# Kernel tuning notes

Measured on AMD Instinct MI355X. Metric: run time of the kernel, lower is better.

Reference implementation:

```python
import jax, jax.numpy as jnp
import numpy as np

FRAME_T = 8
NUM_K = 10


def _masked_att(att, temp):
    # att: [B, H, P, P] -> softmax over groups of size P//FRAME_T, top-k threshold mask
    B, H, P, _ = att.shape
    D = P // FRAME_T
    a = att.reshape(B, H, P, FRAME_T, D)
    a = jax.nn.softmax(a / temp, axis=-1)
    # k-th largest value per row as threshold (torch.topk values are sorted desc)
    margin = jax.lax.top_k(a, NUM_K)[0][..., -1]  # [B,H,P,FRAME_T]
    a = a * (a >= margin[..., None])
    return a  # [B,H,P,FRAME_T,D]


def setup_inputs() -> dict:
    key = jax.random.key(0)
    k1, k2, k3, k4 = jax.random.split(key, 4)
    B, H, P, hd = 4, 12, 1568, 64
    return {
        "att_s": jax.random.normal(k1, (B, H, P, P), dtype=jnp.float32),
        "att_t": jax.random.normal(k2, (B, H, P, P), dtype=jnp.float32),
        "v_s": jax.random.normal(k3, (B, H, P, hd), dtype=jnp.float32),
        "v_t": jax.random.normal(k4, (B, H, P, hd), dtype=jnp.float32),
    }


def reference(att_s, att_t, v_s, v_t):
    temp = jnp.float32(1.0)
    B, H, P, _ = att_t.shape
    H_s = att_s.shape[1]
    h_dim = v_t.shape[-1]
    D = P // FRAME_T

    a_s = _masked_att(att_s, temp)  # [B,Hs,P,T,D]
    a_t = _masked_att(att_t, temp)  # [B,H,P,T,D]

    vt = v_t.reshape(B, H, D, FRAME_T, h_dim)
    vs = v_s.reshape(B, H_s, D, FRAME_T, h_dim)

    norm_s = a_s.sum(-1)  # [B,Hs,P,T]
    norm_t = a_t.sum(-1)

    o_s = jnp.einsum('bhptd,bhdte->bhpte', a_s, vs) / norm_s[..., None]
    o_t = jnp.einsum('bhptd,bhdte->bhpte', a_t, vt) / norm_t[..., None]

    loss = jnp.mean((o_s - o_t) ** 2)
    return loss
```

## Files before the change

### kernel.cpp

```cpp
#include <hip/hip_runtime.h>
#include <hip/hip_bf16.h>

#define PP 1568
#define TT 8
#define DD 196
#define HD 64
#define NBH 48
#define NROW (NBH*PP*TT)
#define RPB 32
#define NBLK3 (NROW/RPB)
#define NRED1 ((NBLK3+255)/256)
#define SUB (8*DD*4)
#define VSLAB (DD*TT*HD)
#define BPB 392
#define KMASK 0xFFFFFF00u

typedef float f4 __attribute__((ext_vector_type(4)));
typedef unsigned u4v __attribute__((ext_vector_type(4)));

__device__ __forceinline__ float readlane_f(float v, int l) {
    return __int_as_float(__builtin_amdgcn_readlane(__float_as_int(v), l));
}

__device__ __forceinline__ float wave_sum_u(float v) {
#define STEPS(ctrl) { float t_ = __int_as_float(__builtin_amdgcn_update_dpp( \
        0, __float_as_int(v), ctrl, 0xF, 0xF, true)); v += t_; }
    STEPS(0x111) STEPS(0x112) STEPS(0x114) STEPS(0x118) STEPS(0x142) STEPS(0x143)
#undef STEPS
    return readlane_f(v, 63);
}

__device__ __forceinline__ unsigned UMX(unsigned a, unsigned b){ return a>b?a:b; }
__device__ __forceinline__ unsigned UMN(unsigned a, unsigned b){ return a<b?a:b; }

__device__ __forceinline__ unsigned med3u(unsigned a, unsigned b, unsigned c) {
    unsigned d;
    asm("v_med3_u32 %0, %1, %2, %3" : "=v"(d) : "v"(a), "v"(b), "v"(c));
    return d;
}

__device__ __forceinline__ float untr(unsigned u) {
    return (u & 0x80000000u) ? __uint_as_float(u ^ 0x80000000u)
                             : __uint_as_float(~u);
}

struct K6  { unsigned k0,k1,k2,k3,k4,k5; };
struct K10 { unsigned k0,k1,k2,k3,k4,k5,k6,k7,k8,k9; };
struct MR  { K10 f; unsigned mx; };

#define PUTK6(Q,X,D) { unsigned b_=__float_as_uint(X); \
  unsigned u_=b_^((unsigned)((int)b_>>31)|0x80000000u); \
  unsigned c_=(u_&KMASK)|(unsigned)(D); \
  unsigned n0_=UMX(Q.k0,c_); \
  unsigned n1_=med3u(Q.k0,Q.k1,c_); \
  unsigned n2_=med3u(Q.k1,Q.k2,c_); \
  unsigned n3_=med3u(Q.k2,Q.k3,c_); \
  unsigned n4_=med3u(Q.k3,Q.k4,c_); \
  unsigned n5_=med3u(Q.k4,Q.k5,c_); \
  Q.k0=n0_; Q.k1=n1_; Q.k2=n2_; Q.k3=n3_; Q.k4=n4_; Q.k5=n5_; }
#define PUT4K6(Q,V,D0) PUTK6(Q,(V).x,(D0)) PUTK6(Q,(V).y,(D0)+1) \
                       PUTK6(Q,(V).z,(D0)+2) PUTK6(Q,(V).w,(D0)+3)

__device__ __forceinline__ K6 chain_rows(const char* stg, int a, int b8) {
    K6 q = {0,0,0,0,0,0};
    const char* rb = stg + a*784 + b8*16;
    f4 v;
    v = *(const f4*)(rb);       PUT4K6(q, v, b8*4)
    v = *(const f4*)(rb+128);   PUT4K6(q, v, b8*4+32)
    v = *(const f4*)(rb+256);   PUT4K6(q, v, b8*4+64)
    v = *(const f4*)(rb+384);   PUT4K6(q, v, b8*4+96)
    v = *(const f4*)(rb+512);   PUT4K6(q, v, b8*4+128)
    v = *(const f4*)(rb+640);   PUT4K6(q, v, b8*4+160)
    if (b8 == 7) { v = *(const f4*)(stg + a*784 + 768); PUT4K6(q, v, 192) }
    return q;
}

#define SWZ(x, pat) (unsigned)__builtin_amdgcn_ds_swizzle((int)(x), pat)
__device__ __forceinline__ K6 kshuf8_6(K6 a) {
    K6 r;
    r.k0=SWZ(a.k0,0x201F); r.k1=SWZ(a.k1,0x201F); r.k2=SWZ(a.k2,0x201F);
    r.k3=SWZ(a.k3,0x201F); r.k4=SWZ(a.k4,0x201F); r.k5=SWZ(a.k5,0x201F);
    return r;
}
__device__ __forceinline__ K10 kshuf16(K10 a) {
    K10 r;
    r.k0=SWZ(a.k0,0x401F); r.k1=SWZ(a.k1,0x401F); r.k2=SWZ(a.k2,0x401F);
    r.k3=SWZ(a.k3,0x401F); r.k4=SWZ(a.k4,0x401F); r.k5=SWZ(a.k5,0x401F);
    r.k6=SWZ(a.k6,0x401F); r.k7=SWZ(a.k7,0x401F); r.k8=SWZ(a.k8,0x401F);
    r.k9=SWZ(a.k9,0x401F);
    return r;
}
__device__ __forceinline__ K10 kbp32(K10 a, int bpx) {
    K10 r;
    r.k0=(unsigned)__builtin_amdgcn_ds_bpermute(bpx,(int)a.k0);
    r.k1=(unsigned)__builtin_amdgcn_ds_bpermute(bpx,(int)a.k1);
    r.k2=(unsigned)__builtin_amdgcn_ds_bpermute(bpx,(int)a.k2);
    r.k3=(unsigned)__builtin_amdgcn_ds_bpermute(bpx,(int)a.k3);
    r.k4=(unsigned)__builtin_amdgcn_ds_bpermute(bpx,(int)a.k4);
    r.k5=(unsigned)__builtin_amdgcn_ds_bpermute(bpx,(int)a.k5);
    r.k6=(unsigned)__builtin_amdgcn_ds_bpermute(bpx,(int)a.k6);
    r.k7=(unsigned)__builtin_amdgcn_ds_bpermute(bpx,(int)a.k7);
    r.k8=(unsigned)__builtin_amdgcn_ds_bpermute(bpx,(int)a.k8);
    r.k9=(unsigned)__builtin_amdgcn_ds_bpermute(bpx,(int)a.k9);
    return r;
}

__device__ __forceinline__ K10 kmrg66(K6 A, K6 B) {
    unsigned p00=UMN(A.k0,B.k0);
    unsigned p01=UMN(A.k0,B.k1), p10=UMN(A.k1,B.k0);
    unsigned p02=UMN(A.k0,B.k2), p11=UMN(A.k1,B.k1), p20=UMN(A.k2,B.k0);
    unsigned p03=UMN(A.k0,B.k3), p12=UMN(A.k1,B.k2), p21=UMN(A.k2,B.k1), p30=UMN(A.k3,B.k0);
    unsigned p04=UMN(A.k0,B.k4), p13=UMN(A.k1,B.k3), p22=UMN(A.k2,B.k2), p31=UMN(A.k3,B.k1), p40=UMN(A.k4,B.k0);
    unsigned p05=UMN(A.k0,B.k5), p14=UMN(A.k1,B.k4), p23=UMN(A.k2,B.k3), p32=UMN(A.k3,B.k2), p41=UMN(A.k4,B.k1), p50=UMN(A.k5,B.k0);
    unsigned p15=UMN(A.k1,B.k5), p24=UMN(A.k2,B.k4), p33=UMN(A.k3,B.k3), p42=UMN(A.k4,B.k2), p51=UMN(A.k5,B.k1);
    unsigned p25=UMN(A.k2,B.k5), p34=UMN(A.k3,B.k4), p43=UMN(A.k4,B.k3), p52=UMN(A.k5,B.k2);
    unsigned p35=UMN(A.k3,B.k5), p44=UMN(A.k4,B.k4), p53=UMN(A.k5,B.k3);
    K10 M;
    M.k0=UMX(A.k0,B.k0);
    M.k1=UMX(UMX(A.k1,B.k1),p00);
    M.k2=UMX(UMX(A.k2,B.k2),UMX(p01,p10));
    M.k3=UMX(UMX(A.k3,B.k3),UMX(p02,UMX(p11,p20)));
    M.k4=UMX(UMX(A.k4,B.k4),UMX(UMX(p03,p12),UMX(p21,p30)));
    M.k5=UMX(UMX(A.k5,B.k5),UMX(UMX(p04,p13),UMX(p22,UMX(p31,p40))));
    M.k6=UMX(UMX(p05,p14),UMX(UMX(p23,p32),UMX(p41,p50)));
    M.k7=UMX(UMX(p15,p24),UMX(p33,UMX(p42,p51)));
    M.k8=UMX(UMX(p25,p34),UMX(p43,p52));
    M.k9=UMX(p35,UMX(p44,p53));
    return M;
}

__device__ __forceinline__ K10 kmrg(K10 A, K10 B) {
    unsigned p00=UMN(A.k0,B.k0);
    unsigned p01=UMN(A.k0,B.k1), p10=UMN(A.k1,B.k0);
    unsigned p02=UMN(A.k0,B.k2), p11=UMN(A.k1,B.k1), p20=UMN(A.k2,B.k0);
    unsigned p03=UMN(A.k0,B.k3), p12=UMN(A.k1,B.k2), p21=UMN(A.k2,B.k1), p30=UMN(A.k3,B.k0);
    unsigned p04=UMN(A.k0,B.k4), p13=UMN(A.k1,B.k3), p22=UMN(A.k2,B.k2), p31=UMN(A.k3,B.k1), p40=UMN(A.k4,B.k0);
    unsigned p05=UMN(A.k0,B.k5), p14=UMN(A.k1,B.k4), p23=UMN(A.k2,B.k3), p32=UMN(A.k3,B.k2), p41=UMN(A.k4,B.k1), p50=UMN(A.k5,B.k0);
    unsigned p06=UMN(A.k0,B.k6), p15=UMN(A.k1,B.k5), p24=UMN(A.k2,B.k4), p33=UMN(A.k3,B.k3), p42=UMN(A.k4,B.k2), p51=UMN(A.k5,B.k1), p60=UMN(A.k6,B.k0);
    unsigned p07=UMN(A.k0,B.k7), p16=UMN(A.k1,B.k6), p25=UMN(A.k2,B.k5), p34=UMN(A.k3,B.k4), p43=UMN(A.k4,B.k3), p52=UMN(A.k5,B.k2), p61=UMN(A.k6,B.k1), p70=UMN(A.k7,B.k0);
    unsigned p08=UMN(A.k0,B.k8), p17=UMN(A.k1,B.k7), p26=UMN(A.k2,B.k6), p35=UMN(A.k3,B.k5), p44=UMN(A.k4,B.k4), p53=UMN(A.k5,B.k3), p62=UMN(A.k6,B.k2), p71=UMN(A.k7,B.k1), p80=UMN(A.k8,B.k0);
    K10 M;
    M.k0=UMX(A.k0,B.k0);
    M.k1=UMX(UMX(A.k1,B.k1),p00);
    M.k2=UMX(UMX(A.k2,B.k2),UMX(p01,p10));
    M.k3=UMX(UMX(A.k3,B.k3),UMX(p02,UMX(p11,p20)));
    M.k4=UMX(UMX(A.k4,B.k4),UMX(UMX(p03,p12),UMX(p21,p30)));
    M.k5=UMX(UMX(A.k5,B.k5),UMX(UMX(p04,p13),UMX(p22,UMX(p31,p40))));
    M.k6=UMX(UMX(A.k6,B.k6),UMX(UMX(p05,p14),UMX(UMX(p23,p32),UMX(p41,p50))));
    M.k7=UMX(UMX(A.k7,B.k7),UMX(UMX(UMX(p06,p15),UMX(p24,p33)),UMX(UMX(p42,p51),p60)));
    M.k8=UMX(UMX(A.k8,B.k8),UMX(UMX(UMX(p07,p16),UMX(p25,p34)),UMX(UMX(p43,p52),UMX(p61,p70))));
    M.k9=UMX(UMX(A.k9,B.k9),UMX(UMX(UMX(p08,p17),UMX(p26,p35)),UMX(UMX(p44,p53),UMX(UMX(p62,p71),p80))));
    return M;
}

__device__ __forceinline__ MR merge_all(K6 q, int bpx) {
    K10 m = kmrg66(q, kshuf8_6(q));
    K10 n = kmrg(m, kshuf16(m));
    K10 r = kbp32(n, bpx);
    MR out;
    out.mx = UMX(n.k0, r.k0);
    out.f.k0=UMX(n.k0,r.k9); out.f.k1=UMX(n.k1,r.k8); out.f.k2=UMX(n.k2,r.k7);
    out.f.k3=UMX(n.k3,r.k6); out.f.k4=UMX(n.k4,r.k5); out.f.k5=UMX(n.k5,r.k4);
    out.f.k6=UMX(n.k6,r.k3); out.f.k7=UMX(n.k7,r.k2); out.f.k8=UMX(n.k8,r.k1);
    out.f.k9=UMX(n.k9,r.k0);
    return out;
}

#define LOADR(R, P) { const char* p_=(P); \
    R##0=*(const f4*)(p_+lane*16); \
    R##1=*(const f4*)(p_+1024+lane*16); \
    R##2=*(const f4*)(p_+2048+lane*16); \
    R##3=*(const f4*)(p_+3072+lane*16); \
    R##4=*(const f4*)(p_+4096+lane*16); \
    R##5=*(const f4*)(p_+5120+lane*16); \
    if (lane<8) R##6=*(const f4*)(p_+6144+lane*16); }
#define STORER(R) { \
    *(f4*)(stg+lane*16)=R##0; *(f4*)(stg+1024+lane*16)=R##1; \
    *(f4*)(stg+2048+lane*16)=R##2; *(f4*)(stg+3072+lane*16)=R##3; \
    *(f4*)(stg+4096+lane*16)=R##4; *(f4*)(stg+5120+lane*16)=R##5; \
    if (lane<8) *(f4*)(stg+6144+lane*16)=R##6; }

#define PKW(F,K) ((__float_as_uint(F)&KMASK)|((K)&0xFFu))

__global__ __launch_bounds__(64, 4) void vtop_main(
        const float* __restrict__ att_s, const float* __restrict__ att_t,
        const float* __restrict__ v_s,   const float* __restrict__ v_t,
        float* __restrict__ partial) {
    __shared__ f4  stgv[SUB/16];
    __shared__ u4v wbuf[5][RPB];
    char* stg = (char*)stgv;

    int lane = threadIdx.x;
    int blk  = blockIdx.x;
    int a = lane & 7, b8 = lane >> 3;
    int bpx = (lane ^ 32) << 2;

    const char* baseS = (const char*)att_s + (size_t)blk * (RPB*DD*4);
    const char* baseT = (const char*)att_t + (size_t)blk * (RPB*DD*4);

    f4 rs0{},rs1{},rs2{},rs3{},rs4{},rs5{},rs6{};
    f4 rt0{},rt1{},rt2{},rt3{},rt4{},rt5{},rt6{};

    LOADR(rs, baseS)

#pragma unroll 1
    for (int s = 0; s < 4; ++s) {
        STORER(rs)
        LOADR(rt, baseT + s*SUB)
        K6 qS = chain_rows(stg, a, b8);
        MR mS = merge_all(qS, bpx);
        STORER(rt)
        if (s < 3) LOADR(rs, baseS + (s+1)*SUB)
        K6 qT = chain_rows(stg, a, b8);
        MR mT = merge_all(qT, bpx);
        K10 fS = mS.f, fT = mT.f;

        float CS = untr(mS.mx & KMASK), CT = untr(mT.mx & KMASK);
        float wS0=__expf(untr(fS.k0&KMASK)-CS), wS1=__expf(untr(fS.k1&KMASK)-CS),
              wS2=__expf(untr(fS.k2&KMASK)-CS), wS3=__expf(untr(fS.k3&KMASK)-CS),
              wS4=__expf(untr(fS.k4&KMASK)-CS), wS5=__expf(untr(fS.k5&KMASK)-CS),
              wS6=__expf(untr(fS.k6&KMASK)-CS), wS7=__expf(untr(fS.k7&KMASK)-CS),
              wS8=__expf(untr(fS.k8&KMASK)-CS), wS9=__expf(untr(fS.k9&KMASK)-CS);
        float wT0=__expf(untr(fT.k0&KMASK)-CT), wT1=__expf(untr(fT.k1&KMASK)-CT),
              wT2=__expf(untr(fT.k2&KMASK)-CT), wT3=__expf(untr(fT.k3&KMASK)-CT),
              wT4=__expf(untr(fT.k4&KMASK)-CT), wT5=__expf(untr(fT.k5&KMASK)-CT),
              wT6=__expf(untr(fT.k6&KMASK)-CT), wT7=__expf(untr(fT.k7&KMASK)-CT),
              wT8=__expf(untr(fT.k8&KMASK)-CT), wT9=__expf(untr(fT.k9&KMASK)-CT);
        float wsS = (((wS0+wS1)+(wS2+wS3))+((wS4+wS5)+(wS6+wS7)))+(wS8+wS9);
        float wsT = (((wT0+wT1)+(wT2+wT3))+((wT4+wT5)+(wT6+wT7)))+(wT8+wT9);
        float invS =  __builtin_amdgcn_rcpf(wsS);
        float invT = -__builtin_amdgcn_rcpf(wsT);

        if (lane < 8) {
            int row = (s << 3) | lane;
            u4v w;
            w.x=PKW(wS0*invS,fS.k0); w.y=PKW(wS1*invS,fS.k1);
            w.z=PKW(wS2*invS,fS.k2); w.w=PKW(wS3*invS,fS.k3);
            wbuf[0][row]=w;
            w.x=PKW(wS4*invS,fS.k4); w.y=PKW(wS5*invS,fS.k5);
            w.z=PKW(wS6*invS,fS.k6); w.w=PKW(wS7*invS,fS.k7);
            wbuf[1][row]=w;
            w.x=PKW(wS8*invS,fS.k8); w.y=PKW(wS9*invS,fS.k9);
            w.z=PKW(wT0*invT,fT.k0); w.w=PKW(wT1*invT,fT.k1);
            wbuf[2][row]=w;
            w.x=PKW(wT2*invT,fT.k2); w.y=PKW(wT3*invT,fT.k3);
            w.z=PKW(wT4*invT,fT.k4); w.w=PKW(wT5*invT,fT.k5);
            wbuf[3][row]=w;
            w.x=PKW(wT6*invT,fT.k6); w.y=PKW(wT7*invT,fT.k7);
            w.z=PKW(wT8*invT,fT.k8); w.w=PKW(wT9*invT,fT.k9);
            wbuf[4][row]=w;
        }
    }

    int bh = blk / BPB;
    const float* vSb = v_s + (size_t)bh * VSLAB;
    const float* vTb = v_t + (size_t)bh * VSLAB;
    float lacc = 0.f;
#pragma unroll 1
    for (int k = 0; k < RPB; ++k) {
        unsigned base = ((unsigned)(k & 7) << 6) + (unsigned)lane;
        u4v w0v=wbuf[0][k], w1v=wbuf[1][k], w2v=wbuf[2][k],
            w3v=wbuf[3][k], w4v=wbuf[4][k];
        float dsum = 0.f;
#define TRM(U, VB) { unsigned u_=(U); \
        float wf_ = __uint_as_float(u_ & KMASK); \
        dsum = fmaf(wf_, VB[((u_ & 0xFFu) << 9) + base], dsum); }
        TRM(w0v.x, vSb) TRM(w0v.y, vSb) TRM(w0v.z, vSb) TRM(w0v.w, vSb)
        TRM(w1v.x, vSb) TRM(w1v.y, vSb) TRM(w1v.z, vSb) TRM(w1v.w, vSb)
        TRM(w2v.x, vSb) TRM(w2v.y, vSb)
        TRM(w2v.z, vTb) TRM(w2v.w, vTb)
        TRM(w3v.x, vTb) TRM(w3v.y, vTb) TRM(w3v.z, vTb) TRM(w3v.w, vTb)
        TRM(w4v.x, vTb) TRM(w4v.y, vTb) TRM(w4v.z, vTb) TRM(w4v.w, vTb)
#undef TRM
        lacc = fmaf(dsum, dsum, lacc);
    }

    float tot = wave_sum_u(lacc);
    if (lane == 0) partial[blk] = tot;
}

__global__ __launch_bounds__(256) void vtop_reduce1(
        const float* __restrict__ partial, float* __restrict__ p2) {
    int i = blockIdx.x * 256 + threadIdx.x;
    float v = (i < NBLK3) ? partial[i] : 0.f;
    float wtot = wave_sum_u(v);
    __shared__ float sm[4];
    int lane = threadIdx.x & 63, wid = threadIdx.x >> 6;
    if (lane == 0) sm[wid] = wtot;
    __syncthreads();
    if (threadIdx.x == 0) p2[blockIdx.x] = (sm[0] + sm[1]) + (sm[2] + sm[3]);
}

__global__ __launch_bounds__(256) void vtop_reduce2(
        const float* __restrict__ p2, float* __restrict__ out) {
    __shared__ double smd[256];
    double a = 0.0;
    if (threadIdx.x < NRED1) a = (double)p2[threadIdx.x];
    smd[threadIdx.x] = a;
    __syncthreads();
    for (int s = 128; s > 0; s >>= 1) {
        if (threadIdx.x < s) smd[threadIdx.x] += smd[threadIdx.x + s];
        __syncthreads();
    }
    if (threadIdx.x == 0) {
        const double inv_n = 1.0 / ((double)NBH * PP * TT * HD);
        out[0] = (float)(smd[0] * inv_n);
    }
}

extern "C" void kernel_launch(void* const* d_in, const int* in_sizes, int n_in,
                              void* d_out, int out_size, void* d_ws, size_t ws_size,
                              hipStream_t stream) {
    const float* att_s = (const float*)d_in[0];
    const float* att_t = (const float*)d_in[1];
    const float* v_s   = (const float*)d_in[2];
    const float* v_t   = (const float*)d_in[3];
    float* out     = (float*)d_out;
    float* partial = (float*)d_ws;
    float* p2      = (float*)d_ws + NBLK3;

    vtop_main<<<NBLK3, 64, 0, stream>>>(att_s, att_t, v_s, v_t, partial);
    vtop_reduce1<<<NRED1, 256, 0, stream>>>(partial, p2);
    vtop_reduce2<<<1, 256, 0, stream>>>(p2, out);
}
```

Baseline: 350.5 us.

## Read attention rows directly from global memory and pack four waves per block

The LDS staging of attention rows and the register double-buffered prefetch are removed. Each lane now reads its strided row segments straight from global memory inside the top-k chain. Blocks grow from one wave to four independent waves, each with its own weight buffer, and per-wave partials feed the reduction. This drops the LDS round trip and its register cost, in exchange for uncoalesced 16-byte global reads, no explicit prefetch, and reliance on occupancy to hide latency.

```diff
diff --git a/kernel.cpp b/kernel.cpp
--- a/kernel.cpp
+++ b/kernel.cpp
@@ -7,12 +7,16 @@
 #define HD 64
 #define NBH 48
 #define NROW (NBH*PP*TT)
-#define RPB 32
-#define NBLK3 (NROW/RPB)
-#define NRED1 ((NBLK3+255)/256)
+#define RPW 32
+#define WPB 4
+#define ROWS_PB (RPW*WPB)
+#define NBLK4 (NROW/ROWS_PB)
+#define NPART (NBLK4*WPB)
+#define NRED1 ((NPART+255)/256)
 #define SUB (8*DD*4)
+#define WSLAB (RPW*DD*4)
 #define VSLAB (DD*TT*HD)
-#define BPB 392
+#define BPB 98
 #define KMASK 0xFFFFFF00u
 
 typedef float f4 __attribute__((ext_vector_type(4)));
@@ -61,9 +65,9 @@
 #define PUT4K6(Q,V,D0) PUTK6(Q,(V).x,(D0)) PUTK6(Q,(V).y,(D0)+1) \
                        PUTK6(Q,(V).z,(D0)+2) PUTK6(Q,(V).w,(D0)+3)
 
-__device__ __forceinline__ K6 chain_rows(const char* stg, int a, int b8) {
+__device__ __forceinline__ K6 chain_g(const char* base, int a, int b8) {
     K6 q = {0,0,0,0,0,0};
-    const char* rb = stg + a*784 + b8*16;
+    const char* rb = base + a*784 + b8*16;
     f4 v;
     v = *(const f4*)(rb);       PUT4K6(q, v, b8*4)
     v = *(const f4*)(rb+128);   PUT4K6(q, v, b8*4+32)
@@ -71,7 +75,7 @@
     v = *(const f4*)(rb+384);   PUT4K6(q, v, b8*4+96)
     v = *(const f4*)(rb+512);   PUT4K6(q, v, b8*4+128)
     v = *(const f4*)(rb+640);   PUT4K6(q, v, b8*4+160)
-    if (b8 == 7) { v = *(const f4*)(stg + a*784 + 768); PUT4K6(q, v, 192) }
+    if (b8 == 7) { v = *(const f4*)(base + a*784 + 768); PUT4K6(q, v, 192) }
     return q;
 }
 
@@ -166,52 +170,30 @@
     return out;
 }
 
-#define LOADR(R, P) { const char* p_=(P); \
-    R##0=*(const f4*)(p_+lane*16); \
-    R##1=*(const f4*)(p_+1024+lane*16); \
-    R##2=*(const f4*)(p_+2048+lane*16); \
-    R##3=*(const f4*)(p_+3072+lane*16); \
-    R##4=*(const f4*)(p_+4096+lane*16); \
-    R##5=*(const f4*)(p_+5120+lane*16); \
-    if (lane<8) R##6=*(const f4*)(p_+6144+lane*16); }
-#define STORER(R) { \
-    *(f4*)(stg+lane*16)=R##0; *(f4*)(stg+1024+lane*16)=R##1; \
-    *(f4*)(stg+2048+lane*16)=R##2; *(f4*)(stg+3072+lane*16)=R##3; \
-    *(f4*)(stg+4096+lane*16)=R##4; *(f4*)(stg+5120+lane*16)=R##5; \
-    if (lane<8) *(f4*)(stg+6144+lane*16)=R##6; }
-
 #define PKW(F,K) ((__float_as_uint(F)&KMASK)|((K)&0xFFu))
 
-__global__ __launch_bounds__(64, 4) void vtop_main(
+__global__ __launch_bounds__(256, 6) void vtop_main(
         const float* __restrict__ att_s, const float* __restrict__ att_t,
         const float* __restrict__ v_s,   const float* __restrict__ v_t,
         float* __restrict__ partial) {
-    __shared__ f4  stgv[SUB/16];
-    __shared__ u4v wbuf[5][RPB];
-    char* stg = (char*)stgv;
-
-    int lane = threadIdx.x;
-    int blk  = blockIdx.x;
+    __shared__ u4v wbuf[WPB][5][RPW];
+
+    int tid  = threadIdx.x;
+    int wid  = tid >> 6;
+    int lane = tid & 63;
     int a = lane & 7, b8 = lane >> 3;
     int bpx = (lane ^ 32) << 2;
-
-    const char* baseS = (const char*)att_s + (size_t)blk * (RPB*DD*4);
-    const char* baseT = (const char*)att_t + (size_t)blk * (RPB*DD*4);
-
-    f4 rs0{},rs1{},rs2{},rs3{},rs4{},rs5{},rs6{};
-    f4 rt0{},rt1{},rt2{},rt3{},rt4{},rt5{},rt6{};
-
-    LOADR(rs, baseS)
+    int blk  = blockIdx.x;
+    int bh   = blk / BPB;
+
+    const char* baseS = (const char*)att_s + (size_t)blk*(ROWS_PB*DD*4) + wid*WSLAB;
+    const char* baseT = (const char*)att_t + (size_t)blk*(ROWS_PB*DD*4) + wid*WSLAB;
 
 #pragma unroll 1
     for (int s = 0; s < 4; ++s) {
-        STORER(rs)
-        LOADR(rt, baseT + s*SUB)
-        K6 qS = chain_rows(stg, a, b8);
+        K6 qS = chain_g(baseS + s*SUB, a, b8);
         MR mS = merge_all(qS, bpx);
-        STORER(rt)
-        if (s < 3) LOADR(rs, baseS + (s+1)*SUB)
-        K6 qT = chain_rows(stg, a, b8);
+        K6 qT = chain_g(baseT + s*SUB, a, b8);
         MR mT = merge_all(qT, bpx);
         K10 fS = mS.f, fT = mT.f;
 
@@ -236,31 +218,30 @@
             u4v w;
             w.x=PKW(wS0*invS,fS.k0); w.y=PKW(wS1*invS,fS.k1);
             w.z=PKW(wS2*invS,fS.k2); w.w=PKW(wS3*invS,fS.k3);
-            wbuf[0][row]=w;
+            wbuf[wid][0][row]=w;
             w.x=PKW(wS4*invS,fS.k4); w.y=PKW(wS5*invS,fS.k5);
             w.z=PKW(wS6*invS,fS.k6); w.w=PKW(wS7*invS,fS.k7);
-            wbuf[1][row]=w;
+            wbuf[wid][1][row]=w;
             w.x=PKW(wS8*invS,fS.k8); w.y=PKW(wS9*invS,fS.k9);
             w.z=PKW(wT0*invT,fT.k0); w.w=PKW(wT1*invT,fT.k1);
-            wbuf[2][row]=w;
+            wbuf[wid][2][row]=w;
             w.x=PKW(wT2*invT,fT.k2); w.y=PKW(wT3*invT,fT.k3);
             w.z=PKW(wT4*invT,fT.k4); w.w=PKW(wT5*invT,fT.k5);
-            wbuf[3][row]=w;
+            wbuf[wid][3][row]=w;
             w.x=PKW(wT6*invT,fT.k6); w.y=PKW(wT7*invT,fT.k7);
             w.z=PKW(wT8*invT,fT.k8); w.w=PKW(wT9*invT,fT.k9);
-            wbuf[4][row]=w;
+            wbuf[wid][4][row]=w;
         }
     }
 
-    int bh = blk / BPB;
     const float* vSb = v_s + (size_t)bh * VSLAB;
     const float* vTb = v_t + (size_t)bh * VSLAB;
     float lacc = 0.f;
 #pragma unroll 1
-    for (int k = 0; k < RPB; ++k) {
+    for (int k = 0; k < RPW; ++k) {
         unsigned base = ((unsigned)(k & 7) << 6) + (unsigned)lane;
-        u4v w0v=wbuf[0][k], w1v=wbuf[1][k], w2v=wbuf[2][k],
-            w3v=wbuf[3][k], w4v=wbuf[4][k];
+        u4v w0v=wbuf[wid][0][k], w1v=wbuf[wid][1][k], w2v=wbuf[wid][2][k],
+            w3v=wbuf[wid][3][k], w4v=wbuf[wid][4][k];
         float dsum = 0.f;
 #define TRM(U, VB) { unsigned u_=(U); \
         float wf_ = __uint_as_float(u_ & KMASK); \
@@ -276,13 +257,13 @@
     }
 
     float tot = wave_sum_u(lacc);
-    if (lane == 0) partial[blk] = tot;
+    if (lane == 0) partial[blk * WPB + wid] = tot;
 }
 
 __global__ __launch_bounds__(256) void vtop_reduce1(
         const float* __restrict__ partial, float* __restrict__ p2) {
     int i = blockIdx.x * 256 + threadIdx.x;
-    float v = (i < NBLK3) ? partial[i] : 0.f;
+    float v = (i < NPART) ? partial[i] : 0.f;
     float wtot = wave_sum_u(v);
     __shared__ float sm[4];
     int lane = threadIdx.x & 63, wid = threadIdx.x >> 6;
@@ -317,9 +298,9 @@
     const float* v_t   = (const float*)d_in[3];
     float* out     = (float*)d_out;
     float* partial = (float*)d_ws;
-    float* p2      = (float*)d_ws + NBLK3;
-
-    vtop_main<<<NBLK3, 64, 0, stream>>>(att_s, att_t, v_s, v_t, partial);
+    float* p2      = (float*)d_ws + NPART;
+
+    vtop_main<<<NBLK4, 256, 0, stream>>>(att_s, att_t, v_s, v_t, partial);
     vtop_reduce1<<<NRED1, 256, 0, stream>>>(partial, p2);
     vtop_reduce2<<<1, 256, 0, stream>>>(p2, out);
 }
```

After: 602.5 us. +71.9%, slower.

## Pack two waves per block and remap block IDs by XCD for V locality

Applied to the files above, without the earlier changes.

Each block now holds two independent 64-lane waves, each with its own staging and weight buffers. Block indices are remapped so that consecutive logical blocks land on the same XCD, which keeps the V slabs of a given head within one XCD's L2. This aims to cut redundant HBM/L2 traffic for the V gathers and to reduce block launch overhead. It adds doubled LDS per block and drops the explicit occupancy hint of 4.

```diff
diff --git a/kernel.cpp b/kernel.cpp
--- a/kernel.cpp
+++ b/kernel.cpp
@@ -7,12 +7,17 @@
 #define HD 64
 #define NBH 48
 #define NROW (NBH*PP*TT)
-#define RPB 32
-#define NBLK3 (NROW/RPB)
-#define NRED1 ((NBLK3+255)/256)
+#define RPW 32
+#define WPB 2
+#define NWAVE (NROW/RPW)
+#define NBLK5 (NWAVE/WPB)
+#define NXCD 8
+#define CPX (NBLK5/NXCD)
+#define NPART NWAVE
+#define NRED1 ((NPART+255)/256)
 #define SUB (8*DD*4)
 #define VSLAB (DD*TT*HD)
-#define BPB 392
+#define WPBH 392
 #define KMASK 0xFFFFFF00u
 
 typedef float f4 __attribute__((ext_vector_type(4)));
@@ -182,21 +187,26 @@
 
 #define PKW(F,K) ((__float_as_uint(F)&KMASK)|((K)&0xFFu))
 
-__global__ __launch_bounds__(64, 4) void vtop_main(
+__global__ __launch_bounds__(128) void vtop_main(
         const float* __restrict__ att_s, const float* __restrict__ att_t,
         const float* __restrict__ v_s,   const float* __restrict__ v_t,
         float* __restrict__ partial) {
-    __shared__ f4  stgv[SUB/16];
-    __shared__ u4v wbuf[5][RPB];
-    char* stg = (char*)stgv;
-
-    int lane = threadIdx.x;
-    int blk  = blockIdx.x;
+    __shared__ f4  stgv[WPB][SUB/16];
+    __shared__ u4v wbuf[WPB][5][RPW];
+
+    int tid  = threadIdx.x;
+    int wid  = tid >> 6;
+    int lane = tid & 63;
+    char* stg = (char*)&stgv[wid][0];
     int a = lane & 7, b8 = lane >> 3;
     int bpx = (lane ^ 32) << 2;
 
-    const char* baseS = (const char*)att_s + (size_t)blk * (RPB*DD*4);
-    const char* baseT = (const char*)att_t + (size_t)blk * (RPB*DD*4);
+    int blk = (blockIdx.x % NXCD) * CPX + blockIdx.x / NXCD;
+    int gwave = blk * WPB + wid;
+    int bh = gwave / WPBH;
+
+    const char* baseS = (const char*)att_s + (size_t)gwave * (RPW*DD*4);
+    const char* baseT = (const char*)att_t + (size_t)gwave * (RPW*DD*4);
 
     f4 rs0{},rs1{},rs2{},rs3{},rs4{},rs5{},rs6{};
     f4 rt0{},rt1{},rt2{},rt3{},rt4{},rt5{},rt6{};
@@ -236,31 +246,30 @@
             u4v w;
             w.x=PKW(wS0*invS,fS.k0); w.y=PKW(wS1*invS,fS.k1);
             w.z=PKW(wS2*invS,fS.k2); w.w=PKW(wS3*invS,fS.k3);
-            wbuf[0][row]=w;
+            wbuf[wid][0][row]=w;
             w.x=PKW(wS4*invS,fS.k4); w.y=PKW(wS5*invS,fS.k5);
             w.z=PKW(wS6*invS,fS.k6); w.w=PKW(wS7*invS,fS.k7);
-            wbuf[1][row]=w;
+            wbuf[wid][1][row]=w;
             w.x=PKW(wS8*invS,fS.k8); w.y=PKW(wS9*invS,fS.k9);
             w.z=PKW(wT0*invT,fT.k0); w.w=PKW(wT1*invT,fT.k1);
-            wbuf[2][row]=w;
+            wbuf[wid][2][row]=w;
             w.x=PKW(wT2*invT,fT.k2); w.y=PKW(wT3*invT,fT.k3);
             w.z=PKW(wT4*invT,fT.k4); w.w=PKW(wT5*invT,fT.k5);
-            wbuf[3][row]=w;
+            wbuf[wid][3][row]=w;
             w.x=PKW(wT6*invT,fT.k6); w.y=PKW(wT7*invT,fT.k7);
             w.z=PKW(wT8*invT,fT.k8); w.w=PKW(wT9*invT,fT.k9);
-            wbuf[4][row]=w;
+            wbuf[wid][4][row]=w;
         }
     }
 
-    int bh = blk / BPB;
     const float* vSb = v_s + (size_t)bh * VSLAB;
     const float* vTb = v_t + (size_t)bh * VSLAB;
     float lacc = 0.f;
 #pragma unroll 1
-    for (int k = 0; k < RPB; ++k) {
+    for (int k = 0; k < RPW; ++k) {
         unsigned base = ((unsigned)(k & 7) << 6) + (unsigned)lane;
-        u4v w0v=wbuf[0][k], w1v=wbuf[1][k], w2v=wbuf[2][k],
-            w3v=wbuf[3][k], w4v=wbuf[4][k];
+        u4v w0v=wbuf[wid][0][k], w1v=wbuf[wid][1][k], w2v=wbuf[wid][2][k],
+            w3v=wbuf[wid][3][k], w4v=wbuf[wid][4][k];
         float dsum = 0.f;
 #define TRM(U, VB) { unsigned u_=(U); \
         float wf_ = __uint_as_float(u_ & KMASK); \
@@ -276,13 +285,13 @@
     }
 
     float tot = wave_sum_u(lacc);
-    if (lane == 0) partial[blk] = tot;
+    if (lane == 0) partial[gwave] = tot;
 }
 
 __global__ __launch_bounds__(256) void vtop_reduce1(
         const float* __restrict__ partial, float* __restrict__ p2) {
     int i = blockIdx.x * 256 + threadIdx.x;
-    float v = (i < NBLK3) ? partial[i] : 0.f;
+    float v = (i < NPART) ? partial[i] : 0.f;
     float wtot = wave_sum_u(v);
     __shared__ float sm[4];
     int lane = threadIdx.x & 63, wid = threadIdx.x >> 6;
@@ -317,9 +326,9 @@
     const float* v_t   = (const float*)d_in[3];
     float* out     = (float*)d_out;
     float* partial = (float*)d_ws;
-    float* p2      = (float*)d_ws + NBLK3;
-
-    vtop_main<<<NBLK3, 64, 0, stream>>>(att_s, att_t, v_s, v_t, partial);
+    float* p2      = (float*)d_ws + NPART;
+
+    vtop_main<<<NBLK5, 128, 0, stream>>>(att_s, att_t, v_s, v_t, partial);
     vtop_reduce1<<<NRED1, 256, 0, stream>>>(partial, p2);
     vtop_reduce2<<<1, 256, 0, stream>>>(p2, out);
 }
```

Result: faster. 331.0 us (-5.5%).
